# Performance work log

Measured on AMD Instinct MI355X. Metric: run time of the kernel, lower is better.

Reference implementation:

```python
import jax, jax.numpy as jnp
import numpy as np

D_MODEL, D_K, D_V, H = 1024, 64, 64, 16
B, NQ, NK = 4, 1024, 1024
HID = D_MODEL // 2


def _dwg(x, W1, b1, W2, b2):
    # DynamicWeightGenerator: sigmoid(fc2(relu(fc1(x))))
    h = jax.nn.relu(jnp.einsum('bnd,hd->bnh', x, W1) + b1)
    return jax.nn.sigmoid(jnp.einsum('bnh,dh->bnd', h, W2) + b2)


def setup_inputs() -> dict:
    key = jax.random.key(0)
    ks = jax.random.split(key, 32)
    s = 0.02
    inp = {
        'queries': jax.random.normal(ks[0], (B, NQ, D_MODEL), jnp.float32),
        'keys': jax.random.normal(ks[1], (B, NK, D_MODEL), jnp.float32),
        'values': jax.random.normal(ks[2], (B, NK, D_MODEL), jnp.float32),
        'attention_mask': jax.random.randint(ks[3], (B, 1, NQ, NK), 0, 2) > 0,
        'attention_weights': jax.random.uniform(ks[4], (B, H, NQ, NK), jnp.float32),
        'memory': jax.random.normal(ks[5], (B, NK), jnp.float32),
        # projections (torch Linear convention: y = x @ W.T + b)
        'Wq': jax.random.normal(ks[6], (H * D_K, D_MODEL), jnp.float32) * s,
        'bq': jnp.zeros((H * D_K,), jnp.float32),
        'Wk': jax.random.normal(ks[7], (H * D_K, D_MODEL), jnp.float32) * s,
        'bk': jnp.zeros((H * D_K,), jnp.float32),
        'Wv': jax.random.normal(ks[8], (H * D_V, D_MODEL), jnp.float32) * s,
        'bv': jnp.zeros((H * D_V,), jnp.float32),
        'Wo': jax.random.normal(ks[9], (D_MODEL, H * D_V), jnp.float32) * s,
        'bo': jnp.zeros((D_MODEL,), jnp.float32),
        'Wmm': jax.random.normal(ks[10], (H * D_V, 1), jnp.float32) * s,
        'bmm': jnp.zeros((H * D_V,), jnp.float32),
    }
    for i, tag in enumerate(['q', 'k', 'v']):
        k0, k1 = ks[11 + 2 * i], ks[12 + 2 * i]
        inp[f'W1{tag}'] = jax.random.normal(k0, (HID, D_MODEL), jnp.float32) * s
        inp[f'b1{tag}'] = jnp.zeros((HID,), jnp.float32)
        inp[f'W2{tag}'] = jax.random.normal(k1, (D_MODEL, HID), jnp.float32) * s
        inp[f'b2{tag}'] = jnp.zeros((D_MODEL,), jnp.float32)
    return inp


def reference(queries, keys, values, attention_mask, attention_weights, memory,
              Wq, bq, Wk, bk, Wv, bv, Wo, bo, Wmm, bmm,
              W1q, b1q, W2q, b2q, W1k, b1k, W2k, b2k, W1v, b1v, W2v, b2v):
    b_s, nq = queries.shape[:2]
    nk = keys.shape[1]
    # dynamic elementwise gating of inputs
    q_in = queries * _dwg(queries, W1q, b1q, W2q, b2q)
    k_in = keys * _dwg(keys, W1k, b1k, W2k, b2k)
    v_in = values * _dwg(values, W1v, b1v, W2v, b2v)
    # projections -> (b, h, n, d)
    q = (jnp.einsum('bnd,ed->bne', q_in, Wq) + bq).reshape(b_s, nq, H, D_K).transpose(0, 2, 1, 3)
    k = (jnp.einsum('bnd,ed->bne', k_in, Wk) + bk).reshape(b_s, nk, H, D_K).transpose(0, 2, 1, 3)
    v = (jnp.einsum('bnd,ed->bne', v_in, Wv) + bv).reshape(b_s, nk, H, D_V).transpose(0, 2, 1, 3)
    # per-token memory factor: fc_mm(memory[..., None]) -> (b, h, nk, d_k)
    mm = (memory[..., None] * Wmm[:, 0] + bmm).reshape(b_s, nk, H, D_K).transpose(0, 2, 1, 3)
    att = jnp.einsum('bhqd,bhkd->bhqk', q, k * mm) / np.sqrt(D_K).astype(np.float32)
    att = att * attention_weights                         # custom scaling (slice [:nk] == full)
    att = jnp.where(attention_mask, -jnp.inf, att)        # masked_fill
    att = jax.nn.softmax(att, axis=-1)
    out = jnp.einsum('bhqk,bhkd->bhqd', att, v * mm)      # (b, h, nq, d_v)
    out = out.transpose(0, 2, 1, 3).reshape(b_s, nq, H * D_V)
    return jnp.einsum('bne,de->bnd', out, Wo) + bo
```

## Files before the change

### kernel.cpp

```cpp
#include <hip/hip_runtime.h>
#include <hip/hip_bf16.h>

#define BB    4
#define NN    1024
#define DM    1024
#define HH    16
#define HID   512
#define TT    (BB * NN)

typedef __attribute__((ext_vector_type(8))) short bf16x8;
typedef __attribute__((ext_vector_type(4))) float f32x4;

__device__ __forceinline__ ushort f2bfu(float f) {
    __hip_bfloat16 h = __float2bfloat16(f);
    return __builtin_bit_cast(ushort, h);
}

__device__ __forceinline__ float bfu2f(ushort u) {
    __hip_bfloat16 h = __builtin_bit_cast(__hip_bfloat16, u);
    return __bfloat162float(h);
}

__device__ __forceinline__ f32x4 mfma16(bf16x8 a, bf16x8 b, f32x4 c) {
    return __builtin_amdgcn_mfma_f32_16x16x32_bf16(a, b, c, 0, 0, 0);
}

__device__ __forceinline__ void gll16(const void* g, void* l) {
    __builtin_amdgcn_global_load_lds(
        (const __attribute__((address_space(1))) unsigned int*)g,
        (__attribute__((address_space(3))) unsigned int*)l, 16, 0, 0);
}

#define NSEG 13
struct CvtAll { const float* s[NSEG]; ushort* d[NSEG]; int bound[NSEG]; };

__global__ __launch_bounds__(256) void cvt_detect(
    CvtAll a, int total, const uint4* __restrict__ m, int n16,
    int* __restrict__ flags)
{
    if (blockIdx.x < 2048) {
        int stride = 256 * 2048;
        for (int i = blockIdx.x * 256 + threadIdx.x; i < total; i += stride) {
            const float* sp = a.s[0];
            ushort* dp = a.d[0];
            int base = 0;
            #pragma unroll
            for (int k = 1; k < NSEG; ++k) {
                bool ge = i >= a.bound[k - 1];
                sp = ge ? a.s[k] : sp;
                dp = ge ? a.d[k] : dp;
                base = ge ? a.bound[k - 1] : base;
            }
            int j = i - base;
            float4 v = ((const float4*)sp)[j];
            uint2 o;
            o.x = (unsigned)f2bfu(v.x) | ((unsigned)f2bfu(v.y) << 16);
            o.y = (unsigned)f2bfu(v.z) | ((unsigned)f2bfu(v.w) << 16);
            ((uint2*)dp)[j] = o;
        }
    } else {
        int bid = blockIdx.x - 2048;
        int stride = 256 * 256;
        unsigned hi = 0, lo = 0;
        for (int i = bid * 256 + threadIdx.x; i < n16; i += stride) {
            uint4 v = m[i];
            unsigned o = v.x | v.y | v.z | v.w;
            lo |= o & 0xFFu;
            hi |= o & 0xFFFFFF00u;
        }
        if (hi) atomicOr(&flags[0], 1);
        if (lo) atomicOr(&flags[1], 1);
    }
}

struct GB {
    const ushort* A[3]; const ushort* W[3];
    const float* bias[3]; void* C[3]; const ushort* X[3];
};

template <int EP, int NF>
__global__ __launch_bounds__(256) void gemm_bf16(
    GB gb, int M, int N, int K,
    const float* __restrict__ mem, const float* __restrict__ Wmm,
    const float* __restrict__ bmm)
{
    __shared__ __align__(16) ushort As[2][128 * 64];
    __shared__ __align__(16) ushort Bs[2][NF * 32 * 64];
    const int z = blockIdx.z;
    const ushort* A = gb.A[z];
    const ushort* W = gb.W[z];
    const float* bias = gb.bias[z];
    void* Cout = gb.C[z];
    const ushort* X = gb.X[z];

    const int tid = threadIdx.x;
    const int lane = tid & 63, w = tid >> 6;
    const int lc = lane & 15, lg = lane >> 4;
    const int m0 = blockIdx.x * 128, n0 = blockIdx.y * (NF * 32);
    const int wm = (w >> 1) * 64, wn = (w & 1) * (NF * 16);
    const int srow = lane >> 3, scol = 8 * ((lane & 7) ^ srow);
    const int swl = (lc & 7) << 3;

    f32x4 acc[4][NF];
    #pragma unroll
    for (int i = 0; i < 4; ++i)
        #pragma unroll
        for (int j = 0; j < NF; ++j)
            acc[i][j] = (f32x4){0.f, 0.f, 0.f, 0.f};

    auto stage = [&](int buf, int k0) {
        #pragma unroll
        for (int ci = 0; ci < 4; ++ci) {
            int c = w + ci * 4;
            gll16(&A[(size_t)(m0 + c * 8 + srow) * K + k0 + scol], &As[buf][c * 512]);
            if (c < NF * 4)
                gll16(&W[(size_t)(n0 + c * 8 + srow) * K + k0 + scol], &Bs[buf][c * 512]);
        }
    };

    stage(0, 0);
    stage(1, 64);
    const int nt = K / 64;

    for (int t = 0; t < nt; ++t) {
        const int cur = t & 1;
        if (t < nt - 1) {
            if constexpr (NF == 4) asm volatile("s_waitcnt vmcnt(8)" ::: "memory");
            else                   asm volatile("s_waitcnt vmcnt(6)" ::: "memory");
        } else {
            asm volatile("s_waitcnt vmcnt(0)" ::: "memory");
        }
        __builtin_amdgcn_sched_barrier(0);
        __builtin_amdgcn_s_barrier();

        bf16x8 af[4][2], bfr[NF][2];
        #pragma unroll
        for (int mi = 0; mi < 4; ++mi) {
            int row = wm + mi * 16 + lc;
            af[mi][0] = *(const bf16x8*)&As[cur][row * 64 + ((lg * 8) ^ swl)];
            af[mi][1] = *(const bf16x8*)&As[cur][row * 64 + ((32 + lg * 8) ^ swl)];
        }
        #pragma unroll
        for (int nj = 0; nj < NF; ++nj) {
            int row = wn + nj * 16 + lc;
            bfr[nj][0] = *(const bf16x8*)&Bs[cur][row * 64 + ((lg * 8) ^ swl)];
            bfr[nj][1] = *(const bf16x8*)&Bs[cur][row * 64 + ((32 + lg * 8) ^ swl)];
        }
        asm volatile("s_waitcnt lgkmcnt(0)" ::: "memory");
        __builtin_amdgcn_sched_barrier(0);
        __builtin_amdgcn_s_barrier();

        if (t + 2 < nt) stage(cur, (t + 2) * 64);

        #pragma unroll
        for (int mi = 0; mi < 4; ++mi)
            #pragma unroll
            for (int nj = 0; nj < NF; ++nj) {
                acc[mi][nj] = mfma16(af[mi][0], bfr[nj][0], acc[mi][nj]);
                acc[mi][nj] = mfma16(af[mi][1], bfr[nj][1], acc[mi][nj]);
            }
    }

    #pragma unroll
    for (int nj = 0; nj < NF; ++nj) {
        int e = n0 + wn + nj * 16 + lc;
        float bv = bias[e];
        float wmv = 0.f, bmv = 0.f;
        if (EP == 7) { wmv = Wmm[e]; bmv = bmm[e]; }
        #pragma unroll
        for (int mi = 0; mi < 4; ++mi) {
            int mbase = m0 + wm + mi * 16 + lg * 4;
            if (EP == 7 && z == 2) {
                ushort u[4];
                #pragma unroll
                for (int r = 0; r < 4; ++r) {
                    float v = (acc[mi][nj][r] + bv) * (mem[mbase + r] * wmv + bmv);
                    u[r] = f2bfu(v);
                }
                int bb = mbase >> 10, n = mbase & 1023;
                size_t off = ((size_t)(bb * HH + (e >> 6)) * 64 + (e & 63)) * NN + n;
                uint2 pk;
                pk.x = (unsigned)u[0] | ((unsigned)u[1] << 16);
                pk.y = (unsigned)u[2] | ((unsigned)u[3] << 16);
                *(uint2*)&((ushort*)Cout)[off] = pk;
            } else {
                #pragma unroll
                for (int r = 0; r < 4; ++r) {
                    int m = mbase + r;
                    float v = acc[mi][nj][r] + bv;
                    if (EP == 1) v = fmaxf(v, 0.f);
                    if (EP == 2) v = bfu2f(X[(size_t)m * N + e]) * (1.f / (1.f + __expf(-v)));
                    if (EP == 7) {
                        if (z == 0) v = v * 0.125f;
                        else        v = v * (mem[m] * wmv + bmv);
                    }
                    size_t off = (size_t)m * N + e;
                    if (EP == 4) ((float*)Cout)[off] = v;
                    else         ((ushort*)Cout)[off] = f2bfu(v);
                }
            }
        }
    }
}

__global__ __launch_bounds__(256) void attn_mfma(
    const ushort* __restrict__ qp, const ushort* __restrict__ kp,
    const ushort* __restrict__ vt, const float* __restrict__ aw,
    const void* __restrict__ maskp, const int* __restrict__ mflags,
    ushort* __restrict__ ob)
{
    __shared__ __align__(16) ushort Ks[64 * 64];
    __shared__ __align__(16) ushort Vs[64 * 64];
    __shared__ __align__(16) ushort Ps[64 * 64];
    const int tid = threadIdx.x, lane = tid & 63, w = tid >> 6;
    const int lc = lane & 15, lg = lane >> 4;
    const int bid = blockIdx.x;
    const int swz = (bid & 7) * 128 + (bid >> 3);
    const int qt = swz & 15, bh = swz >> 4;
    const int b = bh >> 4, h = bh & 15;
    const int q0 = qt * 64, wq = w * 16;
    const int mode = mflags[0] ? (mflags[1] ? 1 : 2) : 0;
    const int srow = lane >> 3, scol = 8 * ((lane & 7) ^ srow);
    const int swl = (lc & 7) << 3;

    const ushort* qrow = &qp[(size_t)(b * NN + q0 + wq + lc) * DM + h * 64];
    bf16x8 bq0 = *(const bf16x8*)&qrow[lg * 8];
    bf16x8 bq1 = *(const bf16x8*)&qrow[32 + lg * 8];

    f32x4 oacc[4];
    #pragma unroll
    for (int i = 0; i < 4; ++i) oacc[i] = (f32x4){0.f, 0.f, 0.f, 0.f};
    float psum = 0.f;
    const int q = q0 + wq + lc;
    const float* awrow = aw + ((size_t)bh * NN + q) * NN;
    const size_t mrowo = ((size_t)b * NN + q) * NN;

    float4 awA[4], awB[4];
    uint4 mk4A[4], mk4B[4];
    unsigned mk1A[4], mk1B[4];

    #pragma unroll
    for (int ci = 0; ci < 2; ++ci) {
        int c = w + ci * 4;
        gll16(&kp[(size_t)(b * NN + c * 8 + srow) * DM + h * 64 + scol], &Ks[c * 512]);
        gll16(&vt[((size_t)bh * 64 + c * 8 + srow) * NN + 0 + scol], &Vs[c * 512]);
    }
    #pragma unroll
    for (int mi = 0; mi < 4; ++mi)
        awA[mi] = *(const float4*)&awrow[mi * 16 + lg * 4];
    if (mode == 1) {
        #pragma unroll
        for (int mi = 0; mi < 4; ++mi)
            mk1A[mi] = *(const unsigned*)&((const unsigned char*)maskp)[mrowo + mi * 16 + lg * 4];
    } else {
        #pragma unroll
        for (int mi = 0; mi < 4; ++mi)
            mk4A[mi] = *(const uint4*)((const char*)maskp + 4 * (mrowo + mi * 16 + lg * 4));
    }
    asm volatile("s_waitcnt vmcnt(0)" ::: "memory");
    __builtin_amdgcn_sched_barrier(0);
    __builtin_amdgcn_s_barrier();

#define ATTN_BODY(T, AWC, MK4C, MK1C, AWN, MK4N, MK1N)                          \
    {                                                                           \
        if ((T) < 15) {                  \
            const int kn = ((T) + 1) * 64;                                      \
            _Pragma("unroll")                                                   \
            for (int mi = 0; mi < 4; ++mi)                                      \
                AWN[mi] = *(const float4*)&awrow[kn + mi * 16 + lg * 4];        \
            if (mode == 1) {                                                    \
                _Pragma("unroll")                                               \
                for (int mi = 0; mi < 4; ++mi)                                  \
                    MK1N[mi] = *(const unsigned*)&((const unsigned char*)maskp) \
                                   [mrowo + kn + mi * 16 + lg * 4];             \
            } else {                                                            \
                _Pragma("unroll")                                               \
                for (int mi = 0; mi < 4; ++mi)                                  \
                    MK4N[mi] = *(const uint4*)((const char*)maskp +             \
                                   4 * (mrowo + kn + mi * 16 + lg * 4));        \
            }                                                                   \
            __builtin_amdgcn_sched_barrier(0);                                  \
        }                                                                       \
                                                               \
        f32x4 sacc[4];                                                          \
        __builtin_amdgcn_s_setprio(1);                                          \
        _Pragma("unroll")                                                       \
        for (int mi = 0; mi < 4; ++mi) {                                        \
            int krow = mi * 16 + lc;                                            \
            bf16x8 a0 = *(const bf16x8*)&Ks[krow * 64 + ((lg * 8) ^ swl)];      \
            bf16x8 a1 = *(const bf16x8*)&Ks[krow * 64 + ((32 + lg * 8) ^ swl)]; \
            f32x4 s = (f32x4){0.f, 0.f, 0.f, 0.f};                              \
            s = mfma16(a0, bq0, s);                                             \
            s = mfma16(a1, bq1, s);                                             \
            sacc[mi] = s;                                                       \
        }                                                                       \
        __builtin_amdgcn_s_setprio(0);                                          \
                                 \
        _Pragma("unroll")                                                       \
        for (int mi = 0; mi < 4; ++mi) {                                        \
            unsigned mk[4];                                                     \
            if (mode == 1) {                                                    \
                mk[0] = MK1C[mi] & 0xffu;         mk[1] = (MK1C[mi] >> 8) & 0xffu;  \
                mk[2] = (MK1C[mi] >> 16) & 0xffu; mk[3] = (MK1C[mi] >> 24) & 0xffu; \
            } else if (mode == 0) {                                             \
                mk[0] = MK4C[mi].x; mk[1] = MK4C[mi].y;                         \
                mk[2] = MK4C[mi].z; mk[3] = MK4C[mi].w;                         \
            } else {                                                            \
                mk[0] = MK4C[mi].x != 0; mk[1] = MK4C[mi].y != 0;               \
                mk[2] = MK4C[mi].z != 0; mk[3] = MK4C[mi].w != 0;               \
            }                                                                   \
            const float aww[4] = {AWC[mi].x, AWC[mi].y, AWC[mi].z, AWC[mi].w};  \
            float pv[4];                                                        \
            _Pragma("unroll")                                                   \
            for (int r = 0; r < 4; ++r) {                                       \
                float sv = sacc[mi][r] * aww[r];                                \
                pv[r] = mk[r] ? 0.f : __expf(sv);                               \
                psum += pv[r];                                                  \
            }                                                                   \
            uint2 pk;                                                           \
            pk.x = (unsigned)f2bfu(pv[0]) | ((unsigned)f2bfu(pv[1]) << 16);     \
            pk.y = (unsigned)f2bfu(pv[2]) | ((unsigned)f2bfu(pv[3]) << 16);     \
            *(uint2*)&Ps[(wq + lc) * 64 + ((mi * 16 + lg * 4) ^ swl)] = pk;     \
        }                                                                       \
                                                                        \
        __builtin_amdgcn_s_setprio(1);                                          \
        _Pragma("unroll")                                                       \
        for (int kk = 0; kk < 2; ++kk) {                                        \
            bf16x8 pa = *(const bf16x8*)&Ps[(wq + lc) * 64 + ((kk * 32 + lg * 8) ^ swl)]; \
            _Pragma("unroll")                                                   \
            for (int nj = 0; nj < 4; ++nj) {                                    \
                bf16x8 vb = *(const bf16x8*)&Vs[(nj * 16 + lc) * 64 + ((kk * 32 + lg * 8) ^ swl)]; \
                oacc[nj] = mfma16(pa, vb, oacc[nj]);                            \
            }                                                                   \
        }                                                                       \
        __builtin_amdgcn_s_setprio(0);                                          \
        if ((T) < 15) {                                                         \
            __builtin_amdgcn_s_barrier();         \
            const int kn = ((T) + 1) * 64;                                      \
            _Pragma("unroll")                                                   \
            for (int ci = 0; ci < 2; ++ci) {       \
                int c = w + ci * 4;                                             \
                gll16(&kp[(size_t)(b * NN + kn + c * 8 + srow) * DM + h * 64 + scol], \
                      &Ks[c * 512]);                                            \
                gll16(&vt[((size_t)bh * 64 + c * 8 + srow) * NN + kn + scol],   \
                      &Vs[c * 512]);                                            \
            }                                                                   \
            asm volatile("s_waitcnt vmcnt(0)" ::: "memory");                    \
            __builtin_amdgcn_sched_barrier(0);                                  \
            __builtin_amdgcn_s_barrier();                   \
        }                                                                       \
    }

    for (int tt = 0; tt < 8; ++tt) {
        const int t0 = tt * 2, t1 = tt * 2 + 1;
        ATTN_BODY(t0, awA, mk4A, mk1A, awB, mk4B, mk1B);
        ATTN_BODY(t1, awB, mk4B, mk1B, awA, mk4A, mk1A);
    }
#undef ATTN_BODY

    psum += __shfl_xor(psum, 16);
    psum += __shfl_xor(psum, 32);
    float inv = 1.0f / psum;
    float invr[4];
    #pragma unroll
    for (int r = 0; r < 4; ++r)
        invr[r] = __shfl(inv, (lane & 48) | (lg * 4 + r));

    #pragma unroll
    for (int nj = 0; nj < 4; ++nj)
        #pragma unroll
        for (int r = 0; r < 4; ++r) {
            int qq = q0 + wq + lg * 4 + r;
            float v = oacc[nj][r] * invr[r];
            ob[(size_t)(b * NN + qq) * DM + h * 64 + nj * 16 + lc] = f2bfu(v);
        }
}

extern "C" void kernel_launch(void* const* d_in, const int* in_sizes, int n_in,
                              void* d_out, int out_size, void* d_ws, size_t ws_size,
                              hipStream_t stream) {
    const float* xin_f[3] = {(const float*)d_in[0], (const float*)d_in[1], (const float*)d_in[2]};
    const void*  maskp   = d_in[3];
    const float* aw      = (const float*)d_in[4];
    const float* memv    = (const float*)d_in[5];
    const float* Wp_f[3] = {(const float*)d_in[6], (const float*)d_in[8], (const float*)d_in[10]};
    const float* bp[3]   = {(const float*)d_in[7], (const float*)d_in[9], (const float*)d_in[11]};
    const float* Wo_f  = (const float*)d_in[12];  const float* bo  = (const float*)d_in[13];
    const float* Wmm = (const float*)d_in[14];    const float* bmm = (const float*)d_in[15];
    const float* W1f[3] = {(const float*)d_in[16], (const float*)d_in[20], (const float*)d_in[24]};
    const float* b1a[3] = {(const float*)d_in[17], (const float*)d_in[21], (const float*)d_in[25]};
    const float* W2f[3] = {(const float*)d_in[18], (const float*)d_in[22], (const float*)d_in[26]};
    const float* b2a[3] = {(const float*)d_in[19], (const float*)d_in[23], (const float*)d_in[27]};

    char* p = (char*)d_ws;
    auto alloc = [&](size_t bytes) { char* r = p; p += (bytes + 255) & ~(size_t)255; return r; };
    int*    mflags = (int*)alloc(256);
    ushort* xbf[3]; for (int t = 0; t < 3; ++t) xbf[t] = (ushort*)alloc((size_t)TT * DM * 2);
    ushort* Wpb[3]; for (int t = 0; t < 3; ++t) Wpb[t] = (ushort*)alloc((size_t)DM * DM * 2);
    ushort* Wob  = (ushort*)alloc((size_t)DM * DM * 2);
    ushort* W1b[3]; for (int t = 0; t < 3; ++t) W1b[t] = (ushort*)alloc((size_t)HID * DM * 2);
    ushort* W2b[3]; for (int t = 0; t < 3; ++t) W2b[t] = (ushort*)alloc((size_t)DM * HID * 2);
    ushort* hbuf[3]; for (int t = 0; t < 3; ++t) hbuf[t] = (ushort*)alloc((size_t)TT * HID * 2);
    ushort* xg[3];  for (int t = 0; t < 3; ++t) xg[t] = (ushort*)alloc((size_t)TT * DM * 2);
    ushort* qpb  = (ushort*)alloc((size_t)TT * DM * 2);
    ushort* ksb  = (ushort*)alloc((size_t)TT * DM * 2);
    ushort* vtb  = (ushort*)alloc((size_t)TT * DM * 2);
    ushort* obuf = (ushort*)alloc((size_t)TT * DM * 2);

    hipMemsetAsync(mflags, 0, 8, stream);

    {
        CvtAll a;
        const int S_IN = TT * DM / 4, S_W = DM * DM / 4, S_H = HID * DM / 4;
        int idx = 0, cum = 0;
        auto seg = [&](const float* s, ushort* d, int n) {
            a.s[idx] = s; a.d[idx] = d; cum += n; a.bound[idx] = cum; ++idx;
        };
        for (int t = 0; t < 3; ++t) seg(xin_f[t], xbf[t], S_IN);
        for (int t = 0; t < 3; ++t) seg(Wp_f[t], Wpb[t], S_W);
        seg(Wo_f, Wob, S_W);
        for (int t = 0; t < 3; ++t) seg(W1f[t], W1b[t], S_H);
        for (int t = 0; t < 3; ++t) seg(W2f[t], W2b[t], S_H);
        cvt_detect<<<2304, 256, 0, stream>>>(a, cum, (const uint4*)maskp,
                                             BB * NN * NN / 16, mflags);
    }

    const dim3 blk(256);
    GB g1 = {}, g2 = {}, g3 = {}, g4 = {};
    for (int t = 0; t < 3; ++t) {
        g1.A[t] = xbf[t];  g1.W[t] = W1b[t]; g1.bias[t] = b1a[t]; g1.C[t] = hbuf[t];
        g2.A[t] = hbuf[t]; g2.W[t] = W2b[t]; g2.bias[t] = b2a[t]; g2.C[t] = xg[t]; g2.X[t] = xbf[t];
        g3.A[t] = xg[t];   g3.W[t] = Wpb[t]; g3.bias[t] = bp[t];
    }
    g3.C[0] = qpb; g3.C[1] = ksb; g3.C[2] = vtb;
    g4.A[0] = obuf; g4.W[0] = Wob; g4.bias[0] = bo; g4.C[0] = d_out;

    gemm_bf16<1, 2><<<dim3(TT / 128, HID / 64, 3), blk, 0, stream>>>(g1, TT, HID, DM, nullptr, nullptr, nullptr);
    gemm_bf16<2, 2><<<dim3(TT / 128, DM / 64, 3), blk, 0, stream>>>(g2, TT, DM, HID, nullptr, nullptr, nullptr);
    gemm_bf16<7, 2><<<dim3(TT / 128, DM / 64, 3), blk, 0, stream>>>(g3, TT, DM, DM, memv, Wmm, bmm);

    attn_mfma<<<dim3(1024), blk, 0, stream>>>(qpb, ksb, vtb, aw,
                                              maskp, mflags, obuf);

    gemm_bf16<4, 2><<<dim3(TT / 128, DM / 64, 1), blk, 0, stream>>>(g4, TT, DM, DM, nullptr, nullptr, nullptr);
}
```

Measured before the change: 263.9 us.

## Split attention over key range into four partial blocks with a combine kernel

The attention kernel now splits the 1024-key range into four chunks, launching four times as many blocks. Each block writes unnormalized fp32 partial outputs and row sums. A new combine kernel adds the partials, normalizes them and writes the bf16 output. This is meant to raise parallelism and shorten each block's serial loop. In exchange it adds substantial fp32 scratch traffic and an extra launch, and it reuses dead input and hidden buffers as scratch space.

```diff
diff --git a/kernel.cpp b/kernel.cpp
--- a/kernel.cpp
+++ b/kernel.cpp
@@ -7,6 +7,8 @@
 #define HH    16
 #define HID   512
 #define TT    (BB * NN)
+#define NSPLIT 4
+#define NTILE  (16 / NSPLIT)
 
 typedef __attribute__((ext_vector_type(8))) short bf16x8;
 typedef __attribute__((ext_vector_type(4))) float f32x4;
@@ -203,11 +205,13 @@
     }
 }
 
-__global__ __launch_bounds__(256) void attn_mfma(
+struct OPS { float* o[NSPLIT]; float* ps; };
+
+__global__ __launch_bounds__(256) void attn_split(
     const ushort* __restrict__ qp, const ushort* __restrict__ kp,
     const ushort* __restrict__ vt, const float* __restrict__ aw,
     const void* __restrict__ maskp, const int* __restrict__ mflags,
-    ushort* __restrict__ ob)
+    OPS ops)
 {
     __shared__ __align__(16) ushort Ks[64 * 64];
     __shared__ __align__(16) ushort Vs[64 * 64];
@@ -215,10 +219,13 @@
     const int tid = threadIdx.x, lane = tid & 63, w = tid >> 6;
     const int lc = lane & 15, lg = lane >> 4;
     const int bid = blockIdx.x;
-    const int swz = (bid & 7) * 128 + (bid >> 3);
+    const int split = bid >> 10;
+    const int inner = bid & 1023;
+    const int swz = (inner & 7) * 128 + (inner >> 3);
     const int qt = swz & 15, bh = swz >> 4;
     const int b = bh >> 4, h = bh & 15;
     const int q0 = qt * 64, wq = w * 16;
+    const int KB = split * NTILE;
     const int mode = mflags[0] ? (mflags[1] ? 1 : 2) : 0;
     const int srow = lane >> 3, scol = 8 * ((lane & 7) ^ srow);
     const int swl = (lc & 7) << 3;
@@ -239,23 +246,26 @@
     uint4 mk4A[4], mk4B[4];
     unsigned mk1A[4], mk1B[4];
 
-    #pragma unroll
-    for (int ci = 0; ci < 2; ++ci) {
-        int c = w + ci * 4;
-        gll16(&kp[(size_t)(b * NN + c * 8 + srow) * DM + h * 64 + scol], &Ks[c * 512]);
-        gll16(&vt[((size_t)bh * 64 + c * 8 + srow) * NN + 0 + scol], &Vs[c * 512]);
-    }
-    #pragma unroll
-    for (int mi = 0; mi < 4; ++mi)
-        awA[mi] = *(const float4*)&awrow[mi * 16 + lg * 4];
-    if (mode == 1) {
+    {
+        const int k0 = KB * 64;
+        #pragma unroll
+        for (int ci = 0; ci < 2; ++ci) {
+            int c = w + ci * 4;
+            gll16(&kp[(size_t)(b * NN + k0 + c * 8 + srow) * DM + h * 64 + scol], &Ks[c * 512]);
+            gll16(&vt[((size_t)bh * 64 + c * 8 + srow) * NN + k0 + scol], &Vs[c * 512]);
+        }
         #pragma unroll
         for (int mi = 0; mi < 4; ++mi)
-            mk1A[mi] = *(const unsigned*)&((const unsigned char*)maskp)[mrowo + mi * 16 + lg * 4];
-    } else {
-        #pragma unroll
-        for (int mi = 0; mi < 4; ++mi)
-            mk4A[mi] = *(const uint4*)((const char*)maskp + 4 * (mrowo + mi * 16 + lg * 4));
+            awA[mi] = *(const float4*)&awrow[k0 + mi * 16 + lg * 4];
+        if (mode == 1) {
+            #pragma unroll
+            for (int mi = 0; mi < 4; ++mi)
+                mk1A[mi] = *(const unsigned*)&((const unsigned char*)maskp)[mrowo + k0 + mi * 16 + lg * 4];
+        } else {
+            #pragma unroll
+            for (int mi = 0; mi < 4; ++mi)
+                mk4A[mi] = *(const uint4*)((const char*)maskp + 4 * (mrowo + k0 + mi * 16 + lg * 4));
+        }
     }
     asm volatile("s_waitcnt vmcnt(0)" ::: "memory");
     __builtin_amdgcn_sched_barrier(0);
@@ -263,8 +273,8 @@
 
 #define ATTN_BODY(T, AWC, MK4C, MK1C, AWN, MK4N, MK1N)                          \
     {                                                                           \
-        if ((T) < 15) {                  \
-            const int kn = ((T) + 1) * 64;                                      \
+        if ((T) < NTILE - 1) {                                                  \
+            const int kn = (KB + (T) + 1) * 64;                                 \
             _Pragma("unroll")                                                   \
             for (int mi = 0; mi < 4; ++mi)                                      \
                 AWN[mi] = *(const float4*)&awrow[kn + mi * 16 + lg * 4];        \
@@ -281,7 +291,6 @@
             }                                                                   \
             __builtin_amdgcn_sched_barrier(0);                                  \
         }                                                                       \
-                                                               \
         f32x4 sacc[4];                                                          \
         __builtin_amdgcn_s_setprio(1);                                          \
         _Pragma("unroll")                                                       \
@@ -295,7 +304,6 @@
             sacc[mi] = s;                                                       \
         }                                                                       \
         __builtin_amdgcn_s_setprio(0);                                          \
-                                 \
         _Pragma("unroll")                                                       \
         for (int mi = 0; mi < 4; ++mi) {                                        \
             unsigned mk[4];                                                     \
@@ -322,7 +330,6 @@
             pk.y = (unsigned)f2bfu(pv[2]) | ((unsigned)f2bfu(pv[3]) << 16);     \
             *(uint2*)&Ps[(wq + lc) * 64 + ((mi * 16 + lg * 4) ^ swl)] = pk;     \
         }                                                                       \
-                                                                        \
         __builtin_amdgcn_s_setprio(1);                                          \
         _Pragma("unroll")                                                       \
         for (int kk = 0; kk < 2; ++kk) {                                        \
@@ -334,11 +341,11 @@
             }                                                                   \
         }                                                                       \
         __builtin_amdgcn_s_setprio(0);                                          \
-        if ((T) < 15) {                                                         \
-            __builtin_amdgcn_s_barrier();         \
-            const int kn = ((T) + 1) * 64;                                      \
+        if ((T) < NTILE - 1) {                                                  \
+            __builtin_amdgcn_s_barrier();               \
+            const int kn = (KB + (T) + 1) * 64;                                 \
             _Pragma("unroll")                                                   \
-            for (int ci = 0; ci < 2; ++ci) {       \
+            for (int ci = 0; ci < 2; ++ci) {                                    \
                 int c = w + ci * 4;                                             \
                 gll16(&kp[(size_t)(b * NN + kn + c * 8 + srow) * DM + h * 64 + scol], \
                       &Ks[c * 512]);                                            \
@@ -347,11 +354,11 @@
             }                                                                   \
             asm volatile("s_waitcnt vmcnt(0)" ::: "memory");                    \
             __builtin_amdgcn_sched_barrier(0);                                  \
-            __builtin_amdgcn_s_barrier();                   \
+            __builtin_amdgcn_s_barrier();                  \
         }                                                                       \
     }
 
-    for (int tt = 0; tt < 8; ++tt) {
+    for (int tt = 0; tt < NTILE / 2; ++tt) {
         const int t0 = tt * 2, t1 = tt * 2 + 1;
         ATTN_BODY(t0, awA, mk4A, mk1A, awB, mk4B, mk1B);
         ATTN_BODY(t1, awB, mk4B, mk1B, awA, mk4A, mk1A);
@@ -360,20 +367,42 @@
 
     psum += __shfl_xor(psum, 16);
     psum += __shfl_xor(psum, 32);
-    float inv = 1.0f / psum;
-    float invr[4];
-    #pragma unroll
-    for (int r = 0; r < 4; ++r)
-        invr[r] = __shfl(inv, (lane & 48) | (lg * 4 + r));
-
+    if (lg == 0)
+        ops.ps[((size_t)split * (BB * HH) + bh) * NN + q] = psum;
+
+    float* Op = ops.o[split];
     #pragma unroll
     for (int nj = 0; nj < 4; ++nj)
         #pragma unroll
         for (int r = 0; r < 4; ++r) {
             int qq = q0 + wq + lg * 4 + r;
-            float v = oacc[nj][r] * invr[r];
-            ob[(size_t)(b * NN + qq) * DM + h * 64 + nj * 16 + lc] = f2bfu(v);
-        }
+            Op[(size_t)(b * NN + qq) * DM + h * 64 + nj * 16 + lc] = oacc[nj][r];
+        }
+}
+
+__global__ __launch_bounds__(256) void attn_combine(OPS ops, ushort* __restrict__ ob) {
+    int stride = blockDim.x * gridDim.x;
+    const int total = TT * DM / 4;
+    for (int i = blockIdx.x * blockDim.x + threadIdx.x; i < total; i += stride) {
+        int flat = i * 4;
+        int row = flat >> 10;
+        int col = flat & 1023;
+        int b = row >> 10, q = row & 1023;
+        int bh = b * HH + (col >> 6);
+        float4 o = make_float4(0.f, 0.f, 0.f, 0.f);
+        float pt = 0.f;
+        #pragma unroll
+        for (int s = 0; s < NSPLIT; ++s) {
+            float4 v = *(const float4*)&ops.o[s][(size_t)row * DM + col];
+            o.x += v.x; o.y += v.y; o.z += v.z; o.w += v.w;
+            pt += ops.ps[((size_t)s * (BB * HH) + bh) * NN + q];
+        }
+        float inv = 1.0f / pt;
+        uint2 pk;
+        pk.x = (unsigned)f2bfu(o.x * inv) | ((unsigned)f2bfu(o.y * inv) << 16);
+        pk.y = (unsigned)f2bfu(o.z * inv) | ((unsigned)f2bfu(o.w * inv) << 16);
+        ((uint2*)ob)[i] = pk;
+    }
 }
 
 extern "C" void kernel_launch(void* const* d_in, const int* in_sizes, int n_in,
@@ -406,6 +435,15 @@
     ushort* ksb  = (ushort*)alloc((size_t)TT * DM * 2);
     ushort* vtb  = (ushort*)alloc((size_t)TT * DM * 2);
     ushort* obuf = (ushort*)alloc((size_t)TT * DM * 2);
+    float* Op3 = (float*)alloc((size_t)TT * DM * 4);
+    float* psb = (float*)alloc((size_t)NSPLIT * BB * HH * NN * 4);
+
+    OPS ops;
+    ops.o[0] = (float*)xbf[0];
+    ops.o[1] = (float*)hbuf[0];
+    ops.o[2] = (float*)((char*)hbuf[0] + (size_t)TT * DM * 4);
+    ops.o[3] = Op3;
+    ops.ps   = psb;
 
     hipMemsetAsync(mflags, 0, 8, stream);
 
@@ -439,8 +477,9 @@
     gemm_bf16<2, 2><<<dim3(TT / 128, DM / 64, 3), blk, 0, stream>>>(g2, TT, DM, HID, nullptr, nullptr, nullptr);
     gemm_bf16<7, 2><<<dim3(TT / 128, DM / 64, 3), blk, 0, stream>>>(g3, TT, DM, DM, memv, Wmm, bmm);
 
-    attn_mfma<<<dim3(1024), blk, 0, stream>>>(qpb, ksb, vtb, aw,
-                                              maskp, mflags, obuf);
+    attn_split<<<dim3(1024 * NSPLIT), blk, 0, stream>>>(qpb, ksb, vtb, aw,
+                                                        maskp, mflags, ops);
+    attn_combine<<<dim3(2048), blk, 0, stream>>>(ops, obuf);
 
     gemm_bf16<4, 2><<<dim3(TT / 128, DM / 64, 1), blk, 0, stream>>>(g4, TT, DM, DM, nullptr, nullptr, nullptr);
 }
```

Measured after the change: 297.5 us. 12.7% more time.

## Give each wave a private K/V LDS tile to remove block barriers

Applied to the files above, without the earlier changes.

Each of the four waves now loads its own full copy of the 64x64 K and V tiles into per-wave LDS buffers instead of sharing one cooperatively loaded tile. This removes the workgroup s_barrier calls around each K/V refill, so waves no longer wait on each other. In exchange each wave issues four times the global-to-LDS loads, and LDS use grows from 24KB to 72KB per block, which can lower occupancy and raise L2 and LDS traffic.

```diff
diff --git a/kernel.cpp b/kernel.cpp
--- a/kernel.cpp
+++ b/kernel.cpp
@@ -209,8 +209,8 @@
     const void* __restrict__ maskp, const int* __restrict__ mflags,
     ushort* __restrict__ ob)
 {
-    __shared__ __align__(16) ushort Ks[64 * 64];
-    __shared__ __align__(16) ushort Vs[64 * 64];
+    __shared__ __align__(16) ushort KsA[4][64 * 64];
+    __shared__ __align__(16) ushort VsA[4][64 * 64];
     __shared__ __align__(16) ushort Ps[64 * 64];
     const int tid = threadIdx.x, lane = tid & 63, w = tid >> 6;
     const int lc = lane & 15, lg = lane >> 4;
@@ -223,9 +223,23 @@
     const int srow = lane >> 3, scol = 8 * ((lane & 7) ^ srow);
     const int swl = (lc & 7) << 3;
 
+    ushort* KsW = &KsA[w][0];
+    ushort* VsW = &VsA[w][0];
+
     const ushort* qrow = &qp[(size_t)(b * NN + q0 + wq + lc) * DM + h * 64];
     bf16x8 bq0 = *(const bf16x8*)&qrow[lg * 8];
     bf16x8 bq1 = *(const bf16x8*)&qrow[32 + lg * 8];
+
+    auto stage = [&](int t) {
+        const int k0 = t * 64;
+        #pragma unroll
+        for (int c = 0; c < 8; ++c) {
+            gll16(&kp[(size_t)(b * NN + k0 + c * 8 + srow) * DM + h * 64 + scol],
+                  &KsW[c * 512]);
+            gll16(&vt[((size_t)bh * 64 + c * 8 + srow) * NN + k0 + scol],
+                  &VsW[c * 512]);
+        }
+    };
 
     f32x4 oacc[4];
     #pragma unroll
@@ -239,12 +253,7 @@
     uint4 mk4A[4], mk4B[4];
     unsigned mk1A[4], mk1B[4];
 
-    #pragma unroll
-    for (int ci = 0; ci < 2; ++ci) {
-        int c = w + ci * 4;
-        gll16(&kp[(size_t)(b * NN + c * 8 + srow) * DM + h * 64 + scol], &Ks[c * 512]);
-        gll16(&vt[((size_t)bh * 64 + c * 8 + srow) * NN + 0 + scol], &Vs[c * 512]);
-    }
+    stage(0);
     #pragma unroll
     for (int mi = 0; mi < 4; ++mi)
         awA[mi] = *(const float4*)&awrow[mi * 16 + lg * 4];
@@ -259,7 +268,6 @@
     }
     asm volatile("s_waitcnt vmcnt(0)" ::: "memory");
     __builtin_amdgcn_sched_barrier(0);
-    __builtin_amdgcn_s_barrier();
 
 #define ATTN_BODY(T, AWC, MK4C, MK1C, AWN, MK4N, MK1N)                          \
     {                                                                           \
@@ -281,21 +289,21 @@
             }                                                                   \
             __builtin_amdgcn_sched_barrier(0);                                  \
         }                                                                       \
-                                                               \
+                                               \
         f32x4 sacc[4];                                                          \
         __builtin_amdgcn_s_setprio(1);                                          \
         _Pragma("unroll")                                                       \
         for (int mi = 0; mi < 4; ++mi) {                                        \
             int krow = mi * 16 + lc;                                            \
-            bf16x8 a0 = *(const bf16x8*)&Ks[krow * 64 + ((lg * 8) ^ swl)];      \
-            bf16x8 a1 = *(const bf16x8*)&Ks[krow * 64 + ((32 + lg * 8) ^ swl)]; \
+            bf16x8 a0 = *(const bf16x8*)&KsW[krow * 64 + ((lg * 8) ^ swl)];     \
+            bf16x8 a1 = *(const bf16x8*)&KsW[krow * 64 + ((32 + lg * 8) ^ swl)];\
             f32x4 s = (f32x4){0.f, 0.f, 0.f, 0.f};                              \
             s = mfma16(a0, bq0, s);                                             \
             s = mfma16(a1, bq1, s);                                             \
             sacc[mi] = s;                                                       \
         }                                                                       \
         __builtin_amdgcn_s_setprio(0);                                          \
-                                 \
+                   \
         _Pragma("unroll")                                                       \
         for (int mi = 0; mi < 4; ++mi) {                                        \
             unsigned mk[4];                                                     \
@@ -322,32 +330,25 @@
             pk.y = (unsigned)f2bfu(pv[2]) | ((unsigned)f2bfu(pv[3]) << 16);     \
             *(uint2*)&Ps[(wq + lc) * 64 + ((mi * 16 + lg * 4) ^ swl)] = pk;     \
         }                                                                       \
-                                                                        \
+                                                        \
         __builtin_amdgcn_s_setprio(1);                                          \
         _Pragma("unroll")                                                       \
         for (int kk = 0; kk < 2; ++kk) {                                        \
             bf16x8 pa = *(const bf16x8*)&Ps[(wq + lc) * 64 + ((kk * 32 + lg * 8) ^ swl)]; \
             _Pragma("unroll")                                                   \
             for (int nj = 0; nj < 4; ++nj) {                                    \
-                bf16x8 vb = *(const bf16x8*)&Vs[(nj * 16 + lc) * 64 + ((kk * 32 + lg * 8) ^ swl)]; \
+                bf16x8 vb = *(const bf16x8*)&VsW[(nj * 16 + lc) * 64 + ((kk * 32 + lg * 8) ^ swl)]; \
                 oacc[nj] = mfma16(pa, vb, oacc[nj]);                            \
             }                                                                   \
         }                                                                       \
         __builtin_amdgcn_s_setprio(0);                                          \
         if ((T) < 15) {                                                         \
-            __builtin_amdgcn_s_barrier();         \
-            const int kn = ((T) + 1) * 64;                                      \
-            _Pragma("unroll")                                                   \
-            for (int ci = 0; ci < 2; ++ci) {       \
-                int c = w + ci * 4;                                             \
-                gll16(&kp[(size_t)(b * NN + kn + c * 8 + srow) * DM + h * 64 + scol], \
-                      &Ks[c * 512]);                                            \
-                gll16(&vt[((size_t)bh * 64 + c * 8 + srow) * NN + kn + scol],   \
-                      &Vs[c * 512]);                                            \
-            }                                                                   \
+                            \
+            asm volatile("s_waitcnt lgkmcnt(0)" ::: "memory");                  \
+            __builtin_amdgcn_sched_barrier(0);                                  \
+            stage((T) + 1);                                                     \
             asm volatile("s_waitcnt vmcnt(0)" ::: "memory");                    \
             __builtin_amdgcn_sched_barrier(0);                                  \
-            __builtin_amdgcn_s_barrier();                   \
         }                                                                       \
     }
 
```

Result: slower. 279.5 us (+5.9%).
